# Performance work log

Measured on AMD Instinct MI355X. Metric: run time of the kernel, lower is better.

The kernel has to match this reference:

```python
import jax, jax.numpy as jnp
import numpy as np

D, H = 128, 8
N_NODE, N_SRC = 50000, 100000
E_NBR, E_INC = 800000, 200000


def _seg_softmax(scores, idx, n):
    # scores: [E, H]; segmented softmax over segments given by idx
    mx = jax.ops.segment_max(scores, idx, num_segments=n)
    ex = jnp.exp(scores - mx[idx])
    sm = jax.ops.segment_sum(ex, idx, num_segments=n)
    return ex / (sm[idx] + 1e-12)


def _ln(x, g, b):
    m = jnp.mean(x, -1, keepdims=True)
    v = jnp.mean((x - m) ** 2, -1, keepdims=True)
    return g * (x - m) / jnp.sqrt(v + 1e-5) + b


def setup_inputs() -> dict:
    key = jax.random.key(0)
    ks = jax.random.split(key, 24)
    s = 1.0 / np.sqrt(D)
    inp = {
        'X': jax.random.normal(ks[0], (N_NODE, D), jnp.float32),
        'X_src': jax.random.normal(ks[1], (N_SRC, D), jnp.float32),
        'W_qkv': jax.random.normal(ks[2], (D, 3 * D), jnp.float32) * s,
        'w_bias': jax.random.normal(ks[3], (D, H), jnp.float32) * s,
        'W_gate': jax.random.normal(ks[4], (D, D), jnp.float32) * s,
        'b_gate': jnp.zeros((D,), jnp.float32),
        'W_o': jax.random.normal(ks[5], (D, D), jnp.float32) * s,
        'W_q': jax.random.normal(ks[6], (D, D), jnp.float32) * s,
        'W_kv': jax.random.normal(ks[7], (D, 2 * D), jnp.float32) * s,
        'w_bias_tgt': jax.random.normal(ks[8], (D, H), jnp.float32) * s,
        'w_bias_src': jax.random.normal(ks[9], (D, H), jnp.float32) * s,
        'W_gate_tgt': jax.random.normal(ks[10], (D, D), jnp.float32) * s,
        'b_gate_tgt': jnp.zeros((D,), jnp.float32),
        'W_gate_src': jax.random.normal(ks[11], (D, D), jnp.float32) * s,
        'b_gate_src': jnp.zeros((D,), jnp.float32),
        'W_o2': jax.random.normal(ks[12], (D, D), jnp.float32) * s,
        'ln1_g': jnp.ones((D,), jnp.float32),
        'ln1_b': jnp.zeros((D,), jnp.float32),
        'ln2_g': jnp.ones((D,), jnp.float32),
        'ln2_b': jnp.zeros((D,), jnp.float32),
        'nbr_src': jax.random.randint(ks[13], (E_NBR,), 0, N_NODE),
        'nbr_dst': jax.random.randint(ks[14], (E_NBR,), 0, N_NODE),
        'inc_tgt': jax.random.randint(ks[15], (E_INC,), 0, N_NODE),
        'inc_src': jax.random.randint(ks[16], (E_INC,), 0, N_SRC),
    }
    return inp


def reference(X, X_src, W_qkv, w_bias, W_gate, b_gate, W_o, W_q, W_kv,
              w_bias_tgt, w_bias_src, W_gate_tgt, b_gate_tgt, W_gate_src,
              b_gate_src, W_o2, ln1_g, ln1_b, ln2_g, ln2_b,
              nbr_src, nbr_dst, inc_tgt, inc_src):
    N = X.shape[0]
    dk = D // H
    scale = 1.0 / np.sqrt(dk)

    # --- SparseNeighbourhoodSelfAttn on level-0 cells ---
    qkv = (X @ W_qkv).reshape(N, 3, H, dk)
    Q, K, V = qkv[:, 0], qkv[:, 1], qkv[:, 2]            # [N,H,dk]
    scores = jnp.sum(Q[nbr_src] * K[nbr_dst], -1) * scale + (X @ w_bias)[nbr_src]  # [E,H]
    attn = _seg_softmax(scores, nbr_src, N)
    out = jax.ops.segment_sum(attn[..., None] * V[nbr_dst], nbr_src, num_segments=N)  # [N,H,dk]
    gate = jax.nn.sigmoid(X @ W_gate + b_gate).reshape(N, H, dk)
    sa = (gate * out).reshape(N, D) @ W_o
    h = _ln(X + sa, ln1_g, ln1_b)

    # --- SparseTopologicalCrossAttn from level-1 cells ---
    Qc = (h @ W_q).reshape(N, H, dk)
    kv = (X_src @ W_kv).reshape(-1, 2, H, dk)
    Kc, Vc = kv[:, 0], kv[:, 1]
    sc = (jnp.sum(Qc[inc_tgt] * Kc[inc_src], -1) * scale
          + (h @ w_bias_tgt)[inc_tgt] + (X_src @ w_bias_src)[inc_src])  # [Ei,H]
    attn_c = _seg_softmax(sc, inc_tgt, N)
    g_src = jax.nn.sigmoid(X_src @ W_gate_src + b_gate_src).reshape(-1, H, dk)
    out_c = jax.ops.segment_sum(attn_c[..., None] * (g_src[inc_src] * Vc[inc_src]),
                                inc_tgt, num_segments=N)
    g_tgt = jax.nn.sigmoid(h @ W_gate_tgt + b_gate_tgt).reshape(N, H, dk)
    ca = (g_tgt * out_c).reshape(N, D) @ W_o2
    return _ln(h + ca, ln2_g, ln2_b)
```

## Files before the change

kernel.cpp:

```cpp
#include <hip/hip_runtime.h>
#include <stdint.h>

__device__ __forceinline__ float bf_lo(uint32_t w) { return __uint_as_float(w << 16); }
__device__ __forceinline__ float bf_hi(uint32_t w) { return __uint_as_float(w & 0xffff0000u); }
__device__ __forceinline__ float bfu(uint16_t u) { return __uint_as_float((uint32_t)u << 16); }
__device__ __forceinline__ uint16_t f2bf(float f) {
    uint32_t u = __float_as_uint(f);
    uint32_t r = ((u >> 16) & 1u) + 0x7fffu;
    return (uint16_t)((u + r) >> 16);
}
__device__ __forceinline__ uint32_t pk2bf(float a, float b) {
    return (uint32_t)f2bf(a) | ((uint32_t)f2bf(b) << 16);
}
__device__ __forceinline__ void gload_lds16(const void* g, void* l) {
    __builtin_amdgcn_global_load_lds(
        (const __attribute__((address_space(1))) void*)g,
        (__attribute__((address_space(3))) void*)l, 16, 0, 0);
}

typedef __attribute__((ext_vector_type(8))) short bf16x8;
typedef __attribute__((ext_vector_type(4))) float f32x4;

#define LOG2E 1.4426950408889634f
#define QSC2  (0.25f * LOG2E)

#define M_BF16 0
#define M_QS   1
#define M_SIG  2
#define M_KVIK 3
#define M_KVIV 4
#define M_GV   5
#define M_LN1  6
#define M_LN2  7
#define M_B8   8

struct GemmJob {
    const uint16_t* A; const uint16_t* WT; const float* bias;
    const uint16_t* aux; const void* resid;
    const float* lng; const float* lnb;
    void* out; int M; int mode;
};
struct GemmJobs { GemmJob j[6]; };

__device__ __forceinline__ void stage_tile(const uint16_t* __restrict__ g,
                                           uint16_t* lds, int tid, int wid)
{
#pragma unroll
    for (int it = 0; it < 8; ++it) {
        int idx = it * 256 + tid;
        int r = idx >> 4, c = idx & 15;
        int gc = c ^ (r & 7);
        gload_lds16(g + (size_t)r * 128 + gc * 8,
                    lds + (size_t)(it * 256 + wid * 64) * 8);
    }
}

__global__ __launch_bounds__(256) void multi_gemm_k(GemmJobs jobs)
{
    __shared__ uint16_t As[128 * 128];
    __shared__ uint16_t Ws[128 * 128];
    const GemmJob jb = jobs.j[blockIdx.y];
    const int m0 = blockIdx.x * 128;
    if (m0 >= jb.M) return;
    const int tid = threadIdx.x;
    const int wid = tid >> 6;
    const int lane = tid & 63;
    const int M = jb.M;

    stage_tile(jb.A + (size_t)m0 * 128, As, tid, wid);
    stage_tile(jb.WT, Ws, tid, wid);
    __syncthreads();

    const int wr = wid >> 1, wc = wid & 1;
    const int l15 = lane & 15, l4 = lane >> 4;
    const int mode = jb.mode;

    if (mode == M_B8) {
        f32x4 acc[4];
#pragma unroll
        for (int i = 0; i < 4; i++) acc[i] = (f32x4){0.f, 0.f, 0.f, 0.f};
#pragma unroll
        for (int kk = 0; kk < 4; ++kk) {
            bf16x8 af0;
            {
                int r = l15;
                int cc = (kk * 4 + l4) ^ (r & 7);
                af0 = *(const bf16x8*)(Ws + r * 128 + cc * 8);
            }
#pragma unroll
            for (int mi = 0; mi < 4; ++mi) {
                int r = wr * 64 + mi * 16 + l15;
                int cc = (kk * 4 + l4) ^ (r & 7);
                bf16x8 bf = *(const bf16x8*)(As + r * 128 + cc * 8);
                acc[mi] = __builtin_amdgcn_mfma_f32_16x16x32_bf16(af0, bf, acc[mi], 0, 0, 0);
            }
        }
        if (wc == 0 && l4 < 2) {
#pragma unroll
            for (int mi = 0; mi < 4; ++mi) {
                int gm = m0 + wr * 64 + mi * 16 + l15;
                if (gm < M) {
                    f32x4 v = acc[mi];
                    *(float4*)((float*)jb.out + (size_t)gm * 8 + l4 * 4) =
                        make_float4(v.x, v.y, v.z, v.w);
                }
            }
        }
        return;
    }

    f32x4 acc[4][4];
#pragma unroll
    for (int i = 0; i < 4; i++)
#pragma unroll
        for (int j = 0; j < 4; j++) acc[i][j] = (f32x4){0.f, 0.f, 0.f, 0.f};

#pragma unroll
    for (int kk = 0; kk < 4; ++kk) {
        bf16x8 af[4], bff[4];
#pragma unroll
        for (int ni = 0; ni < 4; ++ni) {
            int r = wc * 64 + ni * 16 + l15;
            int cc = (kk * 4 + l4) ^ (r & 7);
            af[ni] = *(const bf16x8*)(Ws + r * 128 + cc * 8);
        }
#pragma unroll
        for (int mi = 0; mi < 4; ++mi) {
            int r = wr * 64 + mi * 16 + l15;
            int cc = (kk * 4 + l4) ^ (r & 7);
            bff[mi] = *(const bf16x8*)(As + r * 128 + cc * 8);
        }
#pragma unroll
        for (int ni = 0; ni < 4; ++ni)
#pragma unroll
            for (int mi = 0; mi < 4; ++mi)
                acc[ni][mi] = __builtin_amdgcn_mfma_f32_16x16x32_bf16(
                    af[ni], bff[mi], acc[ni][mi], 0, 0, 0);
    }

    if (mode == M_LN1 || mode == M_LN2) {
        __syncthreads();
        float* redS = (float*)Ws;
        float* redQ = redS + 256;
        float ps[4], qs[4];
#pragma unroll
        for (int mi = 0; mi < 4; ++mi) {
            int row = wr * 64 + mi * 16 + l15;
            int gm = m0 + row;
            float sum = 0.f, sq = 0.f;
#pragma unroll
            for (int ni = 0; ni < 4; ++ni) {
                int gn = wc * 64 + ni * 16 + l4 * 4;
                float r0 = 0.f, r1 = 0.f, r2 = 0.f, r3 = 0.f;
                if (gm < M) {
                    if (mode == M_LN1) {
                        float4 rv = *(const float4*)((const float*)jb.resid + (size_t)gm * 128 + gn);
                        r0 = rv.x; r1 = rv.y; r2 = rv.z; r3 = rv.w;
                    } else {
                        ushort4 rv = *(const ushort4*)((const uint16_t*)jb.resid + (size_t)gm * 128 + gn);
                        r0 = bfu(rv.x); r1 = bfu(rv.y); r2 = bfu(rv.z); r3 = bfu(rv.w);
                    }
                }
                f32x4 t = acc[ni][mi];
                t.x += r0; t.y += r1; t.z += r2; t.w += r3;
                acc[ni][mi] = t;
                sum += t.x + t.y + t.z + t.w;
                sq  += t.x * t.x + t.y * t.y + t.z * t.z + t.w * t.w;
            }
            sum += __shfl_xor(sum, 16); sum += __shfl_xor(sum, 32);
            sq  += __shfl_xor(sq, 16);  sq  += __shfl_xor(sq, 32);
            ps[mi] = sum; qs[mi] = sq;
        }
        if (l4 == 0) {
#pragma unroll
            for (int mi = 0; mi < 4; ++mi) {
                int row = wr * 64 + mi * 16 + l15;
                redS[row * 2 + wc] = ps[mi];
                redQ[row * 2 + wc] = qs[mi];
            }
        }
        __syncthreads();
#pragma unroll
        for (int mi = 0; mi < 4; ++mi) {
            int row = wr * 64 + mi * 16 + l15;
            int gm = m0 + row;
            if (gm >= M) continue;
            float S = redS[row * 2] + redS[row * 2 + 1];
            float Q = redQ[row * 2] + redQ[row * 2 + 1];
            float mean = S * (1.f / 128.f);
            float var  = Q * (1.f / 128.f) - mean * mean;
            float rstd = rsqrtf(var + 1e-5f);
#pragma unroll
            for (int ni = 0; ni < 4; ++ni) {
                int gn = wc * 64 + ni * 16 + l4 * 4;
                float4 gg = *(const float4*)(jb.lng + gn);
                float4 bb = *(const float4*)(jb.lnb + gn);
                f32x4 t = acc[ni][mi];
                float o0 = gg.x * (t.x - mean) * rstd + bb.x;
                float o1 = gg.y * (t.y - mean) * rstd + bb.y;
                float o2 = gg.z * (t.z - mean) * rstd + bb.z;
                float o3 = gg.w * (t.w - mean) * rstd + bb.w;
                if (mode == M_LN1) {
                    ushort4 o;
                    o.x = f2bf(o0); o.y = f2bf(o1); o.z = f2bf(o2); o.w = f2bf(o3);
                    *(ushort4*)((uint16_t*)jb.out + (size_t)gm * 128 + gn) = o;
                } else {
                    *(float4*)((float*)jb.out + (size_t)gm * 128 + gn) =
                        make_float4(o0, o1, o2, o3);
                }
            }
        }
        return;
    }

#pragma unroll
    for (int mi = 0; mi < 4; ++mi) {
        int gm = m0 + wr * 64 + mi * 16 + l15;
        if (gm >= M) continue;
#pragma unroll
        for (int ni = 0; ni < 4; ++ni) {
            int gn = wc * 64 + ni * 16 + l4 * 4;
            f32x4 v = acc[ni][mi];
            if (mode == M_SIG || mode == M_GV) {
                float4 bb = *(const float4*)(jb.bias + gn);
                v.x = 1.f / (1.f + __expf(-(v.x + bb.x)));
                v.y = 1.f / (1.f + __expf(-(v.y + bb.y)));
                v.z = 1.f / (1.f + __expf(-(v.z + bb.z)));
                v.w = 1.f / (1.f + __expf(-(v.w + bb.w)));
            }
            if (mode == M_QS) { v.x *= QSC2; v.y *= QSC2; v.z *= QSC2; v.w *= QSC2; }
            if (mode == M_GV) {
                ushort4 vs = *(const ushort4*)(jb.aux + (size_t)gm * 128 + gn);
                v.x *= bfu(vs.x); v.y *= bfu(vs.y); v.z *= bfu(vs.z); v.w *= bfu(vs.w);
            }
            if (mode == M_KVIK || mode == M_KVIV || mode == M_GV) {
                int which = (mode == M_KVIK) ? 0 : 2;
                uint16_t* op = (uint16_t*)jb.out + (size_t)gm * 256 + gn * 2 + which;
                *reinterpret_cast<uint32_t*>(op)     = pk2bf(v.x, v.y);
                *reinterpret_cast<uint32_t*>(op + 4) = pk2bf(v.z, v.w);
            } else {
                ushort4 o;
                o.x = f2bf(v.x); o.y = f2bf(v.y); o.z = f2bf(v.z); o.w = f2bf(v.w);
                *reinterpret_cast<ushort4*>((uint16_t*)jb.out + (size_t)gm * 128 + gn) = o;
            }
        }
    }
}

#define NBKT_MAX 256
#define CAPSHIFT 14
#define BCAP (1 << CAPSHIFT)

#define PREP_CAST_BLKS 2048
#define PREP_WT_BLKS   896

struct WT14 { const float* src[14]; uint16_t* dst[14]; int nc[14]; int coff[14]; };

__global__ __launch_bounds__(256) void prep_k(
    const float* __restrict__ X, uint16_t* __restrict__ Xb, int n1,
    const float* __restrict__ Xs, uint16_t* __restrict__ Xsb, int n2,
    WT14 wt,
    const int* __restrict__ s1, const int* __restrict__ p1,
    const int* __restrict__ s2, const int* __restrict__ p2,
    int* __restrict__ bktcnt, uint2* __restrict__ tmp,
    int E1, int E2, int N, int shift, int nbkt, int chunk)
{
    __shared__ int hist[NBKT_MAX];
    __shared__ int lcur[NBKT_MAX];
    int bx = blockIdx.x;
    int t = threadIdx.x;
    if (bx < PREP_CAST_BLKS) {
        int i = bx * 256 + t;
        int stride = PREP_CAST_BLKS * 256;
        for (; i < n1 + n2; i += stride) {
            float4 v;
            ushort4 o;
            if (i < n1) v = reinterpret_cast<const float4*>(X)[i];
            else        v = reinterpret_cast<const float4*>(Xs)[i - n1];
            o.x = f2bf(v.x); o.y = f2bf(v.y); o.z = f2bf(v.z); o.w = f2bf(v.w);
            if (i < n1) reinterpret_cast<ushort4*>(Xb)[i] = o;
            else        reinterpret_cast<ushort4*>(Xsb)[i - n1] = o;
        }
    } else if (bx < PREP_CAST_BLKS + PREP_WT_BLKS) {
        int pb = bx - PREP_CAST_BLKS;
        int y = pb >> 6, xx = pb & 63;
        const float* W = wt.src[y];
        uint16_t* WT = wt.dst[y];
        int nc = wt.nc[y], coff = wt.coff[y];
        int i = xx * 256 + t;
        int k = i >> 7, n = i & 127;
        float v;
        if (nc == 8) v = (n < 8) ? W[k * 8 + n] * LOG2E : 0.f;
        else         v = W[(size_t)k * nc + coff + n];
        WT[(size_t)n * 128 + k] = f2bf(v);
    } else {
        int bid = bx - (PREP_CAST_BLKS + PREP_WT_BLKS);
        int Et = E1 + E2;
        int base = bid * chunk;
        int end = min(base + chunk, Et);
        for (int i = t; i < nbkt; i += 256) hist[i] = 0;
        __syncthreads();
        for (int i = base + t; i < end; i += 256) {
            int seg = (i < E1) ? s1[i] : N + s2[i - E1];
            atomicAdd(&hist[seg >> shift], 1);
        }
        __syncthreads();
        for (int i = t; i < nbkt; i += 256) {
            int c = hist[i];
            lcur[i] = (i << CAPSHIFT) + (c ? atomicAdd(&bktcnt[i], c) : 0);
        }
        __syncthreads();
        for (int i = base + t; i < end; i += 256) {
            int seg, pay;
            if (i < E1) { seg = s1[i]; pay = p1[i]; }
            else        { seg = N + s2[i - E1]; pay = p2[i - E1]; }
            int p = atomicAdd(&lcur[seg >> shift], 1);
            tmp[p] = make_uint2((uint32_t)seg, (uint32_t)pay);
        }
    }
}

__global__ __launch_bounds__(256) void binD_k(
    const uint2* __restrict__ tmp, const int* __restrict__ bktcnt,
    int* __restrict__ offs, int* __restrict__ ends,
    int* __restrict__ sorted, int NN, int spb)
{
    extern __shared__ int sh[];
    __shared__ int wt[4];
    int b = blockIdx.x, t = threadIdx.x;
    int s0 = b * spb;
    int segs = min(spb, NN - s0);
    int p0 = b << CAPSHIFT;
    int p1 = p0 + bktcnt[b];
    for (int i = t; i < segs; i += 256) sh[i] = 0;
    __syncthreads();
    for (int i = p0 + t; i < p1; i += 256)
        atomicAdd(&sh[(int)tmp[i].x - s0], 1);
    __syncthreads();
    int e_per = (spb + 255) >> 8;
    int loc[4], cv[4]; int ls = 0;
#pragma unroll 4
    for (int j = 0; j < 4; ++j) {
        if (j < e_per) {
            int idx = t * e_per + j;
            int v = (idx < segs) ? sh[idx] : 0;
            loc[j] = ls; cv[j] = v; ls += v;
        }
    }
    int lane = t & 63, w = t >> 6;
    int sc = ls;
#pragma unroll
    for (int o = 1; o < 64; o <<= 1) { int x = __shfl_up(sc, o); if (lane >= o) sc += x; }
    if (lane == 63) wt[w] = sc;
    __syncthreads();
    int add = 0;
    for (int i = 0; i < w; i++) add += wt[i];
    int texcl = add + sc - ls;
#pragma unroll 4
    for (int j = 0; j < 4; ++j) {
        if (j < e_per) {
            int idx = t * e_per + j;
            if (idx < segs) {
                int pos = p0 + texcl + loc[j];
                offs[s0 + idx] = pos;
                ends[s0 + idx] = pos + cv[j];
                sh[idx] = pos;
            }
        }
    }
    __syncthreads();
    for (int i = p0 + t; i < p1; i += 256) {
        uint2 pr = tmp[i];
        int p = atomicAdd(&sh[(int)pr.x - s0], 1);
        sorted[p] = (int)pr.y;
    }
}

#define SSTEP(KV, ACC)                                                           \
    {                                                                            \
        float s = q0 * bf_lo(KV.x) + q1 * bf_hi(KV.x);                           \
        s += __shfl_xor(s, 1); s += __shfl_xor(s, 2); s += __shfl_xor(s, 4);     \
        float w = exp2f(s + bs);                                                 \
        pa##ACC = fmaf(w, bf_lo(KV.y), pa##ACC);                                 \
        pb##ACC = fmaf(w, bf_hi(KV.y), pb##ACC);                                 \
        dn##ACC += w;                                                            \
    }

__global__ __launch_bounds__(128) void self_attn_k(
    const uint16_t* __restrict__ Qb, const uint16_t* __restrict__ kvi,
    const float* __restrict__ bias1,
    const int* __restrict__ offs, const int* __restrict__ ends,
    const int* __restrict__ sdst,
    const uint16_t* __restrict__ g16, uint16_t* __restrict__ Aout, int N)
{
    int lane = threadIdx.x & 63;
    int n = blockIdx.x * 2 + (threadIdx.x >> 6);
    if (n >= N) return;
    const int lane4 = lane * 4;
    uint32_t qw = *reinterpret_cast<const uint32_t*>(Qb + (size_t)n * 128 + 2 * lane);
    float q0 = bf_lo(qw), q1 = bf_hi(qw);
    float bs = bias1[(size_t)n * 8 + (lane >> 3)];
    int e0 = offs[n], e1 = ends[n];
    float dn0 = 0.f, pa0 = 0.f, pb0 = 0.f;
    float dn1 = 0.f, pa1 = 0.f, pb1 = 0.f;
    float dn2 = 0.f, pa2 = 0.f, pb2 = 0.f;
    float dn3 = 0.f, pa3 = 0.f, pb3 = 0.f;
    int e = e0;
    for (; e + 4 <= e1; e += 4) {
        const int* sp = sdst + __builtin_amdgcn_readfirstlane(e);
        int d0 = __builtin_amdgcn_readfirstlane(sp[0]);
        int d1 = __builtin_amdgcn_readfirstlane(sp[1]);
        int d2 = __builtin_amdgcn_readfirstlane(sp[2]);
        int d3 = __builtin_amdgcn_readfirstlane(sp[3]);
        uint2 kv0 = *reinterpret_cast<const uint2*>(kvi + ((size_t)d0 << 8) + lane4);
        uint2 kv1 = *reinterpret_cast<const uint2*>(kvi + ((size_t)d1 << 8) + lane4);
        uint2 kv2 = *reinterpret_cast<const uint2*>(kvi + ((size_t)d2 << 8) + lane4);
        uint2 kv3 = *reinterpret_cast<const uint2*>(kvi + ((size_t)d3 << 8) + lane4);
        SSTEP(kv0, 0) SSTEP(kv1, 1) SSTEP(kv2, 2) SSTEP(kv3, 3)
    }
    for (; e < e1; ++e) {
        int d0 = __builtin_amdgcn_readfirstlane(sdst[__builtin_amdgcn_readfirstlane(e)]);
        uint2 kv0 = *reinterpret_cast<const uint2*>(kvi + ((size_t)d0 << 8) + lane4);
        SSTEP(kv0, 0)
    }
    float den = (dn0 + dn1) + (dn2 + dn3);
    float a0 = (pa0 + pa1) + (pa2 + pa3);
    float a1 = (pb0 + pb1) + (pb2 + pb3);
    float inv = 1.f / (den + 1e-30f);
    uint32_t gw = *reinterpret_cast<const uint32_t*>(g16 + (size_t)n * 128 + 2 * lane);
    a0 *= inv * bf_lo(gw); a1 *= inv * bf_hi(gw);
    *reinterpret_cast<uint32_t*>(Aout + (size_t)n * 128 + 2 * lane) = pk2bf(a0, a1);
}

#define CSTEP(KV, BSS, ACC)                                                      \
    {                                                                            \
        float s = q0 * bf_lo(KV.x) + q1 * bf_hi(KV.x);                           \
        s += __shfl_xor(s, 1); s += __shfl_xor(s, 2); s += __shfl_xor(s, 4);     \
        float w = exp2f(s + bt + BSS);                                           \
        pa##ACC = fmaf(w, bf_lo(KV.y), pa##ACC);                                 \
        pb##ACC = fmaf(w, bf_hi(KV.y), pb##ACC);                                 \
        dn##ACC += w;                                                            \
    }

__global__ __launch_bounds__(128) void cross_attn_k(
    const uint16_t* __restrict__ Qcb, const float* __restrict__ bias_t,
    const uint16_t* __restrict__ kvgi, const float* __restrict__ bias_s,
    const int* __restrict__ offs, const int* __restrict__ ends,
    const int* __restrict__ ssrc,
    const uint16_t* __restrict__ g16, uint16_t* __restrict__ Aout, int N)
{
    int lane = threadIdx.x & 63;
    int n = blockIdx.x * 2 + (threadIdx.x >> 6);
    if (n >= N) return;
    const int lane4 = lane * 4;
    const int head = lane >> 3;
    uint32_t qw = *reinterpret_cast<const uint32_t*>(Qcb + (size_t)n * 128 + 2 * lane);
    float q0 = bf_lo(qw), q1 = bf_hi(qw);
    float bt = bias_t[(size_t)n * 8 + head];
    int e0 = offs[n], e1 = ends[n];
    float dn0 = 0.f, pa0 = 0.f, pb0 = 0.f;
    float dn1 = 0.f, pa1 = 0.f, pb1 = 0.f;
    float dn2 = 0.f, pa2 = 0.f, pb2 = 0.f;
    float dn3 = 0.f, pa3 = 0.f, pb3 = 0.f;
    int e = e0;
    for (; e + 4 <= e1; e += 4) {
        const int* sp = ssrc + __builtin_amdgcn_readfirstlane(e);
        int d0 = __builtin_amdgcn_readfirstlane(sp[0]);
        int d1 = __builtin_amdgcn_readfirstlane(sp[1]);
        int d2 = __builtin_amdgcn_readfirstlane(sp[2]);
        int d3 = __builtin_amdgcn_readfirstlane(sp[3]);
        uint2 kv0 = *reinterpret_cast<const uint2*>(kvgi + ((size_t)d0 << 8) + lane4);
        uint2 kv1 = *reinterpret_cast<const uint2*>(kvgi + ((size_t)d1 << 8) + lane4);
        uint2 kv2 = *reinterpret_cast<const uint2*>(kvgi + ((size_t)d2 << 8) + lane4);
        uint2 kv3 = *reinterpret_cast<const uint2*>(kvgi + ((size_t)d3 << 8) + lane4);
        float bs0 = (bias_s + (size_t)d0 * 8)[head];
        float bs1 = (bias_s + (size_t)d1 * 8)[head];
        float bs2 = (bias_s + (size_t)d2 * 8)[head];
        float bs3 = (bias_s + (size_t)d3 * 8)[head];
        CSTEP(kv0, bs0, 0) CSTEP(kv1, bs1, 1) CSTEP(kv2, bs2, 2) CSTEP(kv3, bs3, 3)
    }
    for (; e < e1; ++e) {
        int d0 = __builtin_amdgcn_readfirstlane(ssrc[__builtin_amdgcn_readfirstlane(e)]);
        uint2 kv0 = *reinterpret_cast<const uint2*>(kvgi + ((size_t)d0 << 8) + lane4);
        float bs0 = (bias_s + (size_t)d0 * 8)[head];
        CSTEP(kv0, bs0, 0)
    }
    float den = (dn0 + dn1) + (dn2 + dn3);
    float a0 = (pa0 + pa1) + (pa2 + pa3);
    float a1 = (pb0 + pb1) + (pb2 + pb3);
    float inv = 1.f / (den + 1e-30f);
    uint32_t gw = *reinterpret_cast<const uint32_t*>(g16 + (size_t)n * 128 + 2 * lane);
    a0 *= inv * bf_lo(gw); a1 *= inv * bf_hi(gw);
    *reinterpret_cast<uint32_t*>(Aout + (size_t)n * 128 + 2 * lane) = pk2bf(a0, a1);
}

static inline size_t smax_(size_t a, size_t b) { return a > b ? a : b; }

extern "C" void kernel_launch(void* const* d_in, const int* in_sizes, int n_in,
                              void* d_out, int out_size, void* d_ws, size_t ws_size,
                              hipStream_t stream)
{
    const float* X          = (const float*)d_in[0];
    const float* Xs         = (const float*)d_in[1];
    const float* W_qkv      = (const float*)d_in[2];
    const float* w_bias     = (const float*)d_in[3];
    const float* W_gate     = (const float*)d_in[4];
    const float* b_gate     = (const float*)d_in[5];
    const float* W_o        = (const float*)d_in[6];
    const float* W_q        = (const float*)d_in[7];
    const float* W_kv       = (const float*)d_in[8];
    const float* w_bias_tgt = (const float*)d_in[9];
    const float* w_bias_src = (const float*)d_in[10];
    const float* W_gate_tgt = (const float*)d_in[11];
    const float* b_gate_tgt = (const float*)d_in[12];
    const float* W_gate_src = (const float*)d_in[13];
    const float* b_gate_src = (const float*)d_in[14];
    const float* W_o2       = (const float*)d_in[15];
    const float* ln1_g      = (const float*)d_in[16];
    const float* ln1_b      = (const float*)d_in[17];
    const float* ln2_g      = (const float*)d_in[18];
    const float* ln2_b      = (const float*)d_in[19];
    const int* nbr_src      = (const int*)d_in[20];
    const int* nbr_dst      = (const int*)d_in[21];
    const int* inc_tgt      = (const int*)d_in[22];
    const int* inc_src      = (const int*)d_in[23];

    const int N  = in_sizes[0] / 128;
    const int NS = in_sizes[1] / 128;
    const int E1 = in_sizes[20];
    const int E2 = in_sizes[22];
    const int Et = E1 + E2;
    const int NN = 2 * N;
    const int Npad  = (N + 127) & ~127;
    const int NSpad = (NS + 127) & ~127;

    int shift = 9;
    while (((NN + (1 << shift) - 1) >> shift) > NBKT_MAX) ++shift;
    const int spb  = 1 << shift;
    const int nbkt = (NN + spb - 1) >> shift;

    char* ws = (char*)d_ws;
    size_t off = 0;
    auto alloc = [&](size_t bytes) -> void* {
        void* p = ws + off;
        off = (off + bytes + 255) & ~(size_t)255;
        return p;
    };

    uint16_t* Xb   = (uint16_t*)alloc((size_t)Npad * 128 * 2);
    uint16_t* Xsb  = (uint16_t*)alloc((size_t)NSpad * 128 * 2);
    uint16_t* WTq  = (uint16_t*)alloc((size_t)384 * 128 * 2);
    uint16_t* WTkv = (uint16_t*)alloc((size_t)256 * 128 * 2);
    uint16_t* WTg  = (uint16_t*)alloc((size_t)128 * 128 * 2);
    uint16_t* WTo  = (uint16_t*)alloc((size_t)128 * 128 * 2);
    uint16_t* WTq2 = (uint16_t*)alloc((size_t)128 * 128 * 2);
    uint16_t* WTgt = (uint16_t*)alloc((size_t)128 * 128 * 2);
    uint16_t* WTgs = (uint16_t*)alloc((size_t)128 * 128 * 2);
    uint16_t* WTo2 = (uint16_t*)alloc((size_t)128 * 128 * 2);
    uint16_t* WTb1 = (uint16_t*)alloc((size_t)128 * 128 * 2);
    uint16_t* WTbt = (uint16_t*)alloc((size_t)128 * 128 * 2);
    uint16_t* WTbs = (uint16_t*)alloc((size_t)128 * 128 * 2);
    size_t s1a = (size_t)Npad * 384 * 2;
    size_t s1b = (size_t)NSpad * 384 * 2;
    size_t s1c = ((size_t)NBKT_MAX << CAPSHIFT) * 8;
    uint16_t* S1 = (uint16_t*)alloc(smax_(smax_(s1a, s1b), s1c));
    uint16_t* Qb   = S1;
    uint16_t* kvi  = S1 + (size_t)Npad * 128;
    uint16_t* kvgi = S1;
    uint16_t* V16  = S1 + (size_t)NSpad * 256;
    uint2*    tmp  = (uint2*)S1;
    uint16_t* g16  = (uint16_t*)alloc((size_t)N * 128 * 2);
    uint16_t* Qcb  = (uint16_t*)alloc((size_t)N * 128 * 2);
    uint16_t* Awo  = (uint16_t*)alloc((size_t)Npad * 128 * 2);
    uint16_t* hb   = (uint16_t*)alloc((size_t)Npad * 128 * 2);
    float*    b8a  = (float*)alloc((size_t)N * 8 * 4);
    float*    b8s  = (float*)alloc((size_t)NS * 8 * 4);
    int* offs   = (int*)alloc((size_t)NN * 4);
    int* ends   = (int*)alloc((size_t)NN * 4);
    int* sorted = (int*)alloc(((size_t)NBKT_MAX << CAPSHIFT) * 4);
    int* bktcnt = (int*)alloc((size_t)NBKT_MAX * 4);
    (void)ws_size; (void)n_in; (void)out_size;

    const int gA  = Npad / 128;
    const int gAs = NSpad / 128;
    const int gW  = (N + 1) / 2;
    const int BINB = 128;
    const int chunk = (Et + BINB - 1) / BINB;

    hipMemsetAsync(bktcnt, 0, (size_t)NBKT_MAX * 4, stream);
    {
        WT14 wt;
        wt.src[0] = W_qkv; wt.dst[0] = WTq;          wt.nc[0] = 384; wt.coff[0] = 0;
        wt.src[1] = W_qkv; wt.dst[1] = WTq + 16384;  wt.nc[1] = 384; wt.coff[1] = 128;
        wt.src[2] = W_qkv; wt.dst[2] = WTq + 32768;  wt.nc[2] = 384; wt.coff[2] = 256;
        wt.src[3] = W_kv;  wt.dst[3] = WTkv;         wt.nc[3] = 256; wt.coff[3] = 0;
        wt.src[4] = W_kv;  wt.dst[4] = WTkv + 16384; wt.nc[4] = 256; wt.coff[4] = 128;
        wt.src[5] = W_gate;     wt.dst[5] = WTg;  wt.nc[5] = 128; wt.coff[5] = 0;
        wt.src[6] = W_o;        wt.dst[6] = WTo;  wt.nc[6] = 128; wt.coff[6] = 0;
        wt.src[7] = W_q;        wt.dst[7] = WTq2; wt.nc[7] = 128; wt.coff[7] = 0;
        wt.src[8] = W_gate_tgt; wt.dst[8] = WTgt; wt.nc[8] = 128; wt.coff[8] = 0;
        wt.src[9] = W_gate_src; wt.dst[9] = WTgs; wt.nc[9] = 128; wt.coff[9] = 0;
        wt.src[10]= W_o2;       wt.dst[10]= WTo2; wt.nc[10]= 128; wt.coff[10]= 0;
        wt.src[11]= w_bias;     wt.dst[11]= WTb1; wt.nc[11]= 8;   wt.coff[11]= 0;
        wt.src[12]= w_bias_tgt; wt.dst[12]= WTbt; wt.nc[12]= 8;   wt.coff[12]= 0;
        wt.src[13]= w_bias_src; wt.dst[13]= WTbs; wt.nc[13]= 8;   wt.coff[13]= 0;
        prep_k<<<PREP_CAST_BLKS + PREP_WT_BLKS + BINB, 256, 0, stream>>>(
            X, Xb, N * 32, Xs, Xsb, NS * 32, wt,
            nbr_src, nbr_dst, inc_tgt, inc_src,
            bktcnt, tmp, E1, E2, N, shift, nbkt, chunk);
    }
    binD_k<<<nbkt, 256, spb * 4, stream>>>(tmp, bktcnt, offs, ends, sorted, NN, spb);

    {
        GemmJobs jb{};
        jb.j[0] = { Xb, WTq,         nullptr, nullptr, nullptr, nullptr, nullptr, Qb,  N, M_QS };
        jb.j[1] = { Xb, WTq + 16384, nullptr, nullptr, nullptr, nullptr, nullptr, kvi, N, M_KVIK };
        jb.j[2] = { Xb, WTq + 32768, nullptr, nullptr, nullptr, nullptr, nullptr, kvi, N, M_KVIV };
        jb.j[3] = { Xb, WTg,         b_gate,  nullptr, nullptr, nullptr, nullptr, g16, N, M_SIG };
        jb.j[4] = { Xb, WTb1,        nullptr, nullptr, nullptr, nullptr, nullptr, b8a, N, M_B8 };
        multi_gemm_k<<<dim3(gA, 5), 256, 0, stream>>>(jb);
    }
    self_attn_k<<<gW, 128, 0, stream>>>(Qb, kvi, b8a, offs, ends, sorted, g16, Awo, N);
    {
        GemmJobs jb{};
        jb.j[0] = { Awo, WTo, nullptr, nullptr, X, ln1_g, ln1_b, hb, N, M_LN1 };
        multi_gemm_k<<<dim3(gA, 1), 256, 0, stream>>>(jb);
    }
    {
        GemmJobs jb{};
        jb.j[0] = { hb,  WTq2,         nullptr,    nullptr, nullptr, nullptr, nullptr, Qcb,  N,  M_QS };
        jb.j[1] = { hb,  WTgt,         b_gate_tgt, nullptr, nullptr, nullptr, nullptr, g16,  N,  M_SIG };
        jb.j[2] = { Xsb, WTkv,         nullptr,    nullptr, nullptr, nullptr, nullptr, kvgi, NS, M_KVIK };
        jb.j[3] = { Xsb, WTkv + 16384, nullptr,    nullptr, nullptr, nullptr, nullptr, V16,  NS, M_BF16 };
        jb.j[4] = { hb,  WTbt,         nullptr,    nullptr, nullptr, nullptr, nullptr, b8a,  N,  M_B8 };
        multi_gemm_k<<<dim3(gAs, 5), 256, 0, stream>>>(jb);
    }
    {
        GemmJobs jb{};
        jb.j[0] = { Xsb, WTgs, b_gate_src, V16, nullptr, nullptr, nullptr, kvgi, NS, M_GV };
        jb.j[1] = { Xsb, WTbs, nullptr, nullptr, nullptr, nullptr, nullptr, b8s,  NS, M_B8 };
        multi_gemm_k<<<dim3(gAs, 2), 256, 0, stream>>>(jb);
    }
    cross_attn_k<<<gW, 128, 0, stream>>>(Qcb, b8a, kvgi, b8s, offs + N, ends + N, sorted, g16, Awo, N);
    {
        GemmJobs jb{};
        jb.j[0] = { Awo, WTo2, nullptr, nullptr, hb, ln2_g, ln2_b, d_out, N, M_LN2 };
        multi_gemm_k<<<dim3(gA, 1), 256, 0, stream>>>(jb);
    }
}
```

Before: 325.5 us.

## Fuse bin-distribution pass into first multi-GEMM launch and rebalance prep blocks

```diff
diff --git a/kernel.cpp b/kernel.cpp
--- a/kernel.cpp
+++ b/kernel.cpp
@@ -33,12 +33,17 @@
 #define M_LN1  6
 #define M_LN2  7
 #define M_B8   8
+#define M_BIND 10
+
+#define NBKT_MAX 512
+#define CAPSHIFT 13
+#define BCAP (1 << CAPSHIFT)
 
 struct GemmJob {
     const uint16_t* A; const uint16_t* WT; const float* bias;
     const uint16_t* aux; const void* resid;
     const float* lng; const float* lnb;
-    void* out; int M; int mode;
+    void* out; int M; int mode; int i0; int i1;
 };
 struct GemmJobs { GemmJob j[6]; };
 
@@ -60,11 +65,72 @@
     __shared__ uint16_t As[128 * 128];
     __shared__ uint16_t Ws[128 * 128];
     const GemmJob jb = jobs.j[blockIdx.y];
-    const int m0 = blockIdx.x * 128;
-    if (m0 >= jb.M) return;
     const int tid = threadIdx.x;
     const int wid = tid >> 6;
     const int lane = tid & 63;
+    const int mode = jb.mode;
+
+    if (mode == M_BIND) {
+        const uint2* tmp   = (const uint2*)jb.A;
+        const int* bktcnt  = (const int*)jb.WT;
+        int* offs          = (int*)jb.bias;
+        int* ends          = (int*)jb.aux;
+        int* sorted        = (int*)jb.resid;
+        const int spb = jb.i0, NN = jb.i1;
+        int* sh  = (int*)As;
+        int* wtb = (int*)Ws;
+        int b = blockIdx.x, t = tid;
+        int s0 = b * spb;
+        if (s0 >= NN) return;
+        int segs = min(spb, NN - s0);
+        int p0 = b << CAPSHIFT;
+        int p1 = p0 + bktcnt[b];
+        for (int i = t; i < segs; i += 256) sh[i] = 0;
+        __syncthreads();
+        for (int i = p0 + t; i < p1; i += 256)
+            atomicAdd(&sh[(int)tmp[i].x - s0], 1);
+        __syncthreads();
+        int e_per = (spb + 255) >> 8;
+        int loc[4], cv[4]; int ls = 0;
+#pragma unroll 4
+        for (int j = 0; j < 4; ++j) {
+            if (j < e_per) {
+                int idx = t * e_per + j;
+                int v = (idx < segs) ? sh[idx] : 0;
+                loc[j] = ls; cv[j] = v; ls += v;
+            }
+        }
+        int sc = ls;
+#pragma unroll
+        for (int o = 1; o < 64; o <<= 1) { int x = __shfl_up(sc, o); if (lane >= o) sc += x; }
+        if (lane == 63) wtb[wid] = sc;
+        __syncthreads();
+        int add = 0;
+        for (int i = 0; i < wid; i++) add += wtb[i];
+        int texcl = add + sc - ls;
+#pragma unroll 4
+        for (int j = 0; j < 4; ++j) {
+            if (j < e_per) {
+                int idx = t * e_per + j;
+                if (idx < segs) {
+                    int pos = p0 + texcl + loc[j];
+                    offs[s0 + idx] = pos;
+                    ends[s0 + idx] = pos + cv[j];
+                    sh[idx] = pos;
+                }
+            }
+        }
+        __syncthreads();
+        for (int i = p0 + t; i < p1; i += 256) {
+            uint2 pr = tmp[i];
+            int p = atomicAdd(&sh[(int)pr.x - s0], 1);
+            sorted[p] = (int)pr.y;
+        }
+        return;
+    }
+
+    const int m0 = blockIdx.x * 128;
+    if (m0 >= jb.M) return;
     const int M = jb.M;
 
     stage_tile(jb.A + (size_t)m0 * 128, As, tid, wid);
@@ -73,7 +139,6 @@
 
     const int wr = wid >> 1, wc = wid & 1;
     const int l15 = lane & 15, l4 = lane >> 4;
-    const int mode = jb.mode;
 
     if (mode == M_B8) {
         f32x4 acc[4];
@@ -247,12 +312,9 @@
     }
 }
 
-#define NBKT_MAX 256
-#define CAPSHIFT 14
-#define BCAP (1 << CAPSHIFT)
-
-#define PREP_CAST_BLKS 2048
+#define PREP_BINA_BLKS 512
 #define PREP_WT_BLKS   896
+#define PREP_CAST_BLKS 1536
 
 struct WT14 { const float* src[14]; uint16_t* dst[14]; int nc[14]; int coff[14]; };
 
@@ -269,20 +331,32 @@
     __shared__ int lcur[NBKT_MAX];
     int bx = blockIdx.x;
     int t = threadIdx.x;
-    if (bx < PREP_CAST_BLKS) {
-        int i = bx * 256 + t;
-        int stride = PREP_CAST_BLKS * 256;
-        for (; i < n1 + n2; i += stride) {
-            float4 v;
-            ushort4 o;
-            if (i < n1) v = reinterpret_cast<const float4*>(X)[i];
-            else        v = reinterpret_cast<const float4*>(Xs)[i - n1];
-            o.x = f2bf(v.x); o.y = f2bf(v.y); o.z = f2bf(v.z); o.w = f2bf(v.w);
-            if (i < n1) reinterpret_cast<ushort4*>(Xb)[i] = o;
-            else        reinterpret_cast<ushort4*>(Xsb)[i - n1] = o;
-        }
-    } else if (bx < PREP_CAST_BLKS + PREP_WT_BLKS) {
-        int pb = bx - PREP_CAST_BLKS;
+    if (bx < PREP_BINA_BLKS) {
+        int bid = bx;
+        int Et = E1 + E2;
+        int base = bid * chunk;
+        int end = min(base + chunk, Et);
+        for (int i = t; i < nbkt; i += 256) hist[i] = 0;
+        __syncthreads();
+        for (int i = base + t; i < end; i += 256) {
+            int seg = (i < E1) ? s1[i] : N + s2[i - E1];
+            atomicAdd(&hist[seg >> shift], 1);
+        }
+        __syncthreads();
+        for (int i = t; i < nbkt; i += 256) {
+            int c = hist[i];
+            lcur[i] = (i << CAPSHIFT) + (c ? atomicAdd(&bktcnt[i], c) : 0);
+        }
+        __syncthreads();
+        for (int i = base + t; i < end; i += 256) {
+            int seg, pay;
+            if (i < E1) { seg = s1[i]; pay = p1[i]; }
+            else        { seg = N + s2[i - E1]; pay = p2[i - E1]; }
+            int p = atomicAdd(&lcur[seg >> shift], 1);
+            tmp[p] = make_uint2((uint32_t)seg, (uint32_t)pay);
+        }
+    } else if (bx < PREP_BINA_BLKS + PREP_WT_BLKS) {
+        int pb = bx - PREP_BINA_BLKS;
         int y = pb >> 6, xx = pb & 63;
         const float* W = wt.src[y];
         uint16_t* WT = wt.dst[y];
@@ -294,85 +368,17 @@
         else         v = W[(size_t)k * nc + coff + n];
         WT[(size_t)n * 128 + k] = f2bf(v);
     } else {
-        int bid = bx - (PREP_CAST_BLKS + PREP_WT_BLKS);
-        int Et = E1 + E2;
-        int base = bid * chunk;
-        int end = min(base + chunk, Et);
-        for (int i = t; i < nbkt; i += 256) hist[i] = 0;
-        __syncthreads();
-        for (int i = base + t; i < end; i += 256) {
-            int seg = (i < E1) ? s1[i] : N + s2[i - E1];
-            atomicAdd(&hist[seg >> shift], 1);
-        }
-        __syncthreads();
-        for (int i = t; i < nbkt; i += 256) {
-            int c = hist[i];
-            lcur[i] = (i << CAPSHIFT) + (c ? atomicAdd(&bktcnt[i], c) : 0);
-        }
-        __syncthreads();
-        for (int i = base + t; i < end; i += 256) {
-            int seg, pay;
-            if (i < E1) { seg = s1[i]; pay = p1[i]; }
-            else        { seg = N + s2[i - E1]; pay = p2[i - E1]; }
-            int p = atomicAdd(&lcur[seg >> shift], 1);
-            tmp[p] = make_uint2((uint32_t)seg, (uint32_t)pay);
-        }
-    }
-}
-
-__global__ __launch_bounds__(256) void binD_k(
-    const uint2* __restrict__ tmp, const int* __restrict__ bktcnt,
-    int* __restrict__ offs, int* __restrict__ ends,
-    int* __restrict__ sorted, int NN, int spb)
-{
-    extern __shared__ int sh[];
-    __shared__ int wt[4];
-    int b = blockIdx.x, t = threadIdx.x;
-    int s0 = b * spb;
-    int segs = min(spb, NN - s0);
-    int p0 = b << CAPSHIFT;
-    int p1 = p0 + bktcnt[b];
-    for (int i = t; i < segs; i += 256) sh[i] = 0;
-    __syncthreads();
-    for (int i = p0 + t; i < p1; i += 256)
-        atomicAdd(&sh[(int)tmp[i].x - s0], 1);
-    __syncthreads();
-    int e_per = (spb + 255) >> 8;
-    int loc[4], cv[4]; int ls = 0;
-#pragma unroll 4
-    for (int j = 0; j < 4; ++j) {
-        if (j < e_per) {
-            int idx = t * e_per + j;
-            int v = (idx < segs) ? sh[idx] : 0;
-            loc[j] = ls; cv[j] = v; ls += v;
-        }
-    }
-    int lane = t & 63, w = t >> 6;
-    int sc = ls;
-#pragma unroll
-    for (int o = 1; o < 64; o <<= 1) { int x = __shfl_up(sc, o); if (lane >= o) sc += x; }
-    if (lane == 63) wt[w] = sc;
-    __syncthreads();
-    int add = 0;
-    for (int i = 0; i < w; i++) add += wt[i];
-    int texcl = add + sc - ls;
-#pragma unroll 4
-    for (int j = 0; j < 4; ++j) {
-        if (j < e_per) {
-            int idx = t * e_per + j;
-            if (idx < segs) {
-                int pos = p0 + texcl + loc[j];
-                offs[s0 + idx] = pos;
-                ends[s0 + idx] = pos + cv[j];
-                sh[idx] = pos;
-            }
-        }
-    }
-    __syncthreads();
-    for (int i = p0 + t; i < p1; i += 256) {
-        uint2 pr = tmp[i];
-        int p = atomicAdd(&sh[(int)pr.x - s0], 1);
-        sorted[p] = (int)pr.y;
+        int i = (bx - PREP_BINA_BLKS - PREP_WT_BLKS) * 256 + t;
+        int stride = PREP_CAST_BLKS * 256;
+        for (; i < n1 + n2; i += stride) {
+            float4 v;
+            ushort4 o;
+            if (i < n1) v = reinterpret_cast<const float4*>(X)[i];
+            else        v = reinterpret_cast<const float4*>(Xs)[i - n1];
+            o.x = f2bf(v.x); o.y = f2bf(v.y); o.z = f2bf(v.z); o.w = f2bf(v.w);
+            if (i < n1) reinterpret_cast<ushort4*>(Xb)[i] = o;
+            else        reinterpret_cast<ushort4*>(Xsb)[i - n1] = o;
+        }
     }
 }
 
@@ -534,7 +540,7 @@
     const int Npad  = (N + 127) & ~127;
     const int NSpad = (NS + 127) & ~127;
 
-    int shift = 9;
+    int shift = 8;
     while (((NN + (1 << shift) - 1) >> shift) > NBKT_MAX) ++shift;
     const int spb  = 1 << shift;
     const int nbkt = (NN + spb - 1) >> shift;
@@ -562,13 +568,12 @@
     uint16_t* WTbs = (uint16_t*)alloc((size_t)128 * 128 * 2);
     size_t s1a = (size_t)Npad * 384 * 2;
     size_t s1b = (size_t)NSpad * 384 * 2;
-    size_t s1c = ((size_t)NBKT_MAX << CAPSHIFT) * 8;
-    uint16_t* S1 = (uint16_t*)alloc(smax_(smax_(s1a, s1b), s1c));
+    uint16_t* S1 = (uint16_t*)alloc(smax_(s1a, s1b));
     uint16_t* Qb   = S1;
     uint16_t* kvi  = S1 + (size_t)Npad * 128;
     uint16_t* kvgi = S1;
     uint16_t* V16  = S1 + (size_t)NSpad * 256;
-    uint2*    tmp  = (uint2*)S1;
+    uint2* tmp  = (uint2*)alloc(((size_t)NBKT_MAX << CAPSHIFT) * 8);
     uint16_t* g16  = (uint16_t*)alloc((size_t)N * 128 * 2);
     uint16_t* Qcb  = (uint16_t*)alloc((size_t)N * 128 * 2);
     uint16_t* Awo  = (uint16_t*)alloc((size_t)Npad * 128 * 2);
@@ -584,8 +589,7 @@
     const int gA  = Npad / 128;
     const int gAs = NSpad / 128;
     const int gW  = (N + 1) / 2;
-    const int BINB = 128;
-    const int chunk = (Et + BINB - 1) / BINB;
+    const int chunk = (Et + PREP_BINA_BLKS - 1) / PREP_BINA_BLKS;
 
     hipMemsetAsync(bktcnt, 0, (size_t)NBKT_MAX * 4, stream);
     {
@@ -604,12 +608,11 @@
         wt.src[11]= w_bias;     wt.dst[11]= WTb1; wt.nc[11]= 8;   wt.coff[11]= 0;
         wt.src[12]= w_bias_tgt; wt.dst[12]= WTbt; wt.nc[12]= 8;   wt.coff[12]= 0;
         wt.src[13]= w_bias_src; wt.dst[13]= WTbs; wt.nc[13]= 8;   wt.coff[13]= 0;
-        prep_k<<<PREP_CAST_BLKS + PREP_WT_BLKS + BINB, 256, 0, stream>>>(
+        prep_k<<<PREP_BINA_BLKS + PREP_WT_BLKS + PREP_CAST_BLKS, 256, 0, stream>>>(
             X, Xb, N * 32, Xs, Xsb, NS * 32, wt,
             nbr_src, nbr_dst, inc_tgt, inc_src,
             bktcnt, tmp, E1, E2, N, shift, nbkt, chunk);
     }
-    binD_k<<<nbkt, 256, spb * 4, stream>>>(tmp, bktcnt, offs, ends, sorted, NN, spb);
 
     {
         GemmJobs jb{};
@@ -618,7 +621,10 @@
         jb.j[2] = { Xb, WTq + 32768, nullptr, nullptr, nullptr, nullptr, nullptr, kvi, N, M_KVIV };
         jb.j[3] = { Xb, WTg,         b_gate,  nullptr, nullptr, nullptr, nullptr, g16, N, M_SIG };
         jb.j[4] = { Xb, WTb1,        nullptr, nullptr, nullptr, nullptr, nullptr, b8a, N, M_B8 };
-        multi_gemm_k<<<dim3(gA, 5), 256, 0, stream>>>(jb);
+        jb.j[5] = { (const uint16_t*)tmp, (const uint16_t*)bktcnt, (const float*)offs,
+                    (const uint16_t*)ends, (const void*)sorted, nullptr, nullptr,
+                    nullptr, 1 << 30, M_BIND, spb, NN };
+        multi_gemm_k<<<dim3(gA, 6), 256, 0, stream>>>(jb);
     }
     self_attn_k<<<gW, 128, 0, stream>>>(Qb, kvi, b8a, offs, ends, sorted, g16, Awo, N);
     {
```

Result: faster. 292.3 us (-10.2%).
